# Optimization experiments

Measured on AMD Instinct MI355X. Metric: run time of the kernel, lower is better.

Reference implementation:

```python
import jax, jax.numpy as jnp
import numpy as np
import math

B, L, IN_DIM, OUT_DIM = 2, 2048, 128, 128
H, DH = 8, 32            # num_heads, dim_head
ED = H * DH * 2          # embed_dim = 512
DEPTH = 1
LAMBDA_INIT = 0.8 - 0.6 * math.exp(-0.3 * (DEPTH + 1))
EPS = 1e-8


def setup_inputs() -> dict:
    key = jax.random.key(0)
    ks = jax.random.split(key, 10)
    x = jax.random.normal(ks[0], (B, 1, L, IN_DIM), dtype=jnp.float32)
    mask_2d = jax.random.bernoulli(ks[1], 0.9, (B, L, L))
    Wq = jax.random.normal(ks[2], (IN_DIM, ED), dtype=jnp.float32) * 0.05
    Wkv = jax.random.normal(ks[3], (IN_DIM, 2 * ED), dtype=jnp.float32) * 0.05
    Wout = jax.random.normal(ks[4], (ED, OUT_DIM), dtype=jnp.float32) * 0.05
    lambda_q1 = jax.random.normal(ks[5], (DH,), dtype=jnp.float32) * 0.1
    lambda_k1 = jax.random.normal(ks[6], (DH,), dtype=jnp.float32) * 0.1
    lambda_q2 = jax.random.normal(ks[7], (DH,), dtype=jnp.float32) * 0.1
    lambda_k2 = jax.random.normal(ks[8], (DH,), dtype=jnp.float32) * 0.1
    gamma = jnp.ones((2 * DH,), dtype=jnp.float32)
    return {"x": x, "mask_2d": mask_2d, "Wq": Wq, "Wkv": Wkv, "Wout": Wout,
            "lambda_q1": lambda_q1, "lambda_k1": lambda_k1,
            "lambda_q2": lambda_q2, "lambda_k2": lambda_k2, "gamma": gamma}


def reference(x, mask_2d, Wq, Wkv, Wout, lambda_q1, lambda_k1, lambda_q2, lambda_k2, gamma):
    b = x.shape[0]
    xs = x[:, 0]                                   # [b, L, in_dim]
    q = xs @ Wq                                    # [b, L, 2*H*DH]
    k, v = jnp.split(xs @ Wkv, 2, axis=-1)
    q = q.reshape(b, L, 2 * H, DH).transpose(0, 2, 1, 3) * (DH ** -0.5)  # [b,2H,L,d]
    k = k.reshape(b, L, 2 * H, DH).transpose(0, 2, 1, 3)                 # [b,2H,L,d]
    v = v.reshape(b, L, H, 2 * DH).transpose(0, 2, 1, 3)                 # [b,H,L,2d]
    dots = jnp.einsum('bnld,bnmd->bnlm', q, k)     # [b,2H,L,L]
    mask_value = -jnp.finfo(dots.dtype).max
    dots = jnp.where(mask_2d[:, None, :, :], dots, mask_value)
    attn_w = jax.nn.softmax(dots.astype(jnp.float32), axis=-1).astype(dots.dtype)
    lam1 = jnp.exp(jnp.sum(lambda_q1 * lambda_k1))
    lam2 = jnp.exp(jnp.sum(lambda_q2 * lambda_k2))
    lam = lam1 - lam2 + LAMBDA_INIT
    attn_w = attn_w.reshape(b, H, 2, L, L)
    attn_w = attn_w[:, :, 0] - lam * attn_w[:, :, 1]   # [b,H,L,L]
    attn = jnp.einsum('bhlm,bhmd->bhld', attn_w, v)    # [b,H,L,2d]
    rms = jnp.sqrt(jnp.mean(attn ** 2, axis=-1, keepdims=True))
    attn = gamma * (attn / (rms + EPS)) * (1.0 - LAMBDA_INIT)
    out = attn.transpose(0, 2, 1, 3).reshape(b, L, H * 2 * DH) @ Wout  # [b,L,out_dim]
    return out[:, None]                             # [b,1,L,out_dim]
```

## Files before the change

### kernel.cpp

```cpp
#include <hip/hip_runtime.h>
#include <float.h>
#include <math.h>

typedef __attribute__((ext_vector_type(8))) short short8;
typedef __attribute__((ext_vector_type(4))) float f32x4;
typedef __attribute__((ext_vector_type(4))) unsigned short ushort4v;

constexpr int SEQL = 2048;
constexpr int NQH  = 16;
constexpr int NVH  = 8;
constexpr int DHD  = 32;
constexpr float LAMB_INIT = 0.4707130183436648f;
constexpr float REPS      = 1e-8f;
constexpr float QW        = 0.25503492f;

static __device__ __forceinline__ unsigned short f2bf(float f) {
    union { float f; unsigned u; } a; a.f = f;
    unsigned u = a.u;
    u += 0x7fffu + ((u >> 16) & 1u);
    return (unsigned short)(u >> 16);
}

static __device__ __forceinline__ unsigned cvtpk(float lo, float hi) {
    unsigned r;
    asm("v_cvt_pk_bf16_f32 %0, %1, %2" : "=v"(r) : "v"(lo), "v"(hi));
    return r;
}

static __device__ __forceinline__ float expv(float x) {
    float r;
    asm("v_exp_f32 %0, %1" : "=v"(r) : "v"(x));
    return r;
}

static __device__ __forceinline__ void stage16(const unsigned short* g, unsigned short* l) {
    __builtin_amdgcn_global_load_lds(
        (const __attribute__((address_space(1))) unsigned int*)g,
        (__attribute__((address_space(3))) unsigned int*)l, 16, 0, 0);
}

__global__ __launch_bounds__(256) void pack_prep_kernel(
        const unsigned char* __restrict__ mb, const int* __restrict__ mi,
        unsigned long long* __restrict__ bits,
        const float* __restrict__ x, const float* __restrict__ Wq,
        const float* __restrict__ Wkv, const float* __restrict__ Wout,
        unsigned short* __restrict__ xb, unsigned short* __restrict__ Wf,
        unsigned short* __restrict__ WfO) {
    __shared__ int cnt[256];
    int t = threadIdx.x;
    int c = 0;
    #pragma unroll
    for (int i = 0; i < 16; ++i) c += (mb[t * 16 + i] != 0);
    cnt[t] = c;
    __syncthreads();
    for (int s = 128; s > 0; s >>= 1) { if (t < s) cnt[t] += cnt[t + s]; __syncthreads(); }
    int f = cnt[0] > 2048;
    int gtid = blockIdx.x * 256 + t;
    int nthr = gridDim.x * 256;
    {
        const int total = 2 * SEQL * (SEQL / 64);
        int wid = blockIdx.x * 4 + (t >> 6);
        int lane = t & 63;
        int stride = gridDim.x * 4;
        for (int w = wid; w < total; w += stride) {
            int e = w * 64 + lane;
            int v = f ? (int)mb[e] : mi[e];
            unsigned long long b = __ballot(v != 0);
            if (lane == 0) bits[w] = b;
        }
    }
    {
        float4 v = ((const float4*)x)[gtid];
        ushort4v o = { f2bf(v.x), f2bf(v.y), f2bf(v.z), f2bf(v.w) };
        ((ushort4v*)xb)[gtid] = o;
    }
    for (int e = gtid; e < 262144; e += nthr) {
        int k = e >> 11, cc = e & 2047;
        if (cc < 1536) {
            float v = (cc < 512) ? Wq[(size_t)k * 512 + cc] * QW
                                 : Wkv[(size_t)k * 1024 + (cc - 512)];
            int cp = cc >> 4, lr = cc & 15, kk = k >> 5, lg = (k >> 3) & 3, j = k & 7;
            Wf[(((size_t)(cp * 4 + kk) * 4 + lg) * 16 + lr) * 8 + j] = f2bf(v);
        }
    }
    if (gtid < 65536) {
        int k = gtid >> 7, cc = gtid & 127;
        float v = Wout[gtid];
        int cp = cc >> 4, lr = cc & 15, kk = k >> 5, lg = (k >> 3) & 3, j = k & 7;
        WfO[(((size_t)(cp * 16 + kk) * 4 + lg) * 16 + lr) * 8 + j] = f2bf(v);
    }
}

__global__ __launch_bounds__(256) void qkv_mfma_kernel(
        const unsigned short* __restrict__ xb, const unsigned short* __restrict__ Wf,
        unsigned short* __restrict__ Q, unsigned short* __restrict__ Kf,
        unsigned short* __restrict__ Vf) {
    int t = threadIdx.x, w = t >> 6, lane = t & 63, lr = lane & 15, lg = lane >> 4;
    int lid = blockIdx.x;
    int swz = (lid & 7) * 192 + (lid >> 3);
    int by = swz >> 6, bx = swz & 63;
    int r0 = bx * 64 + w * 16;
    short8 ax[4];
    #pragma unroll
    for (int kk = 0; kk < 4; ++kk)
        ax[kk] = *(const short8*)(xb + (size_t)(r0 + lr) * 128 + kk * 32 + lg * 8);
    f32x4 acc[4];
    #pragma unroll
    for (int ct = 0; ct < 4; ++ct) acc[ct] = (f32x4){0.f, 0.f, 0.f, 0.f};
    #pragma unroll
    for (int ct = 0; ct < 4; ++ct) {
        int cp = by * 4 + ct;
        #pragma unroll
        for (int kk = 0; kk < 4; ++kk) {
            short8 bw = *(const short8*)(Wf + (size_t)(cp * 4 + kk) * 512 + lane * 8);
            acc[ct] = __builtin_amdgcn_mfma_f32_16x16x32_bf16(ax[kk], bw, acc[ct], 0, 0, 0);
        }
    }
    int gr0 = r0 + 4 * lg;
    int b = gr0 >> 11;
    if (by < 8) {
        #pragma unroll
        for (int ct = 0; ct < 4; ++ct) {
            int col = by * 64 + 16 * ct + lr;
            int n = col >> 5, d = col & 31;
            #pragma unroll
            for (int r = 0; r < 4; ++r) {
                int l = (gr0 + r) & 2047;
                Q[(((size_t)(b * NQH + n)) * SEQL + l) * DHD + d] = f2bf(acc[ct][r]);
            }
        }
    } else if (by < 16) {
        #pragma unroll
        for (int ct = 0; ct < 4; ++ct) {
            int ck = by * 64 + 16 * ct + lr - 512;
            int n = ck >> 5, dk = ck & 31;
            size_t hb = ((size_t)(b * NQH + n)) * 65536 + (dk >> 3) * 128 + (dk & 7);
            #pragma unroll
            for (int r = 0; r < 4; ++r) {
                int l = (gr0 + r) & 2047;
                Kf[hb + (size_t)((l >> 6) * 4 + ((l >> 4) & 3)) * 512 + (l & 15) * 8]
                    = f2bf(acc[ct][r]);
            }
        }
    } else {
        #pragma unroll
        for (int ct = 0; ct < 4; ++ct) {
            int cv = by * 64 + 16 * ct + lr - 1024;
            int h = cv >> 6, d = cv & 63;
            size_t hb = ((size_t)(b * NVH + h)) * 131072 + (d >> 4) * 512 + (d & 15) * 8;
            #pragma unroll
            for (int r = 0; r < 4; ++r) {
                int l = (gr0 + r) & 2047;
                Vf[hb + (size_t)((l >> 6) * 2 + ((l >> 5) & 1)) * 2048
                      + ((l >> 4) & 1) * 4 + ((l >> 2) & 3) * 128 + (l & 3)]
                    = f2bf(acc[ct][r]);
            }
        }
    }
}

__global__ __launch_bounds__(512, 2) void attn_kernel(
        const unsigned short* __restrict__ Q, const unsigned short* __restrict__ Kf,
        const unsigned short* __restrict__ Vf, const unsigned long long* __restrict__ bits,
        const float* __restrict__ lq1, const float* __restrict__ lk1,
        const float* __restrict__ lq2, const float* __restrict__ lk2,
        const float* __restrict__ gamma, unsigned short* __restrict__ Ab) {
    __shared__ unsigned short lds[3][8192];
    int tid = threadIdx.x;
    int w = tid >> 6, lane = tid & 63;
    int lr = lane & 15, lg = lane >> 4;
    int ws = w & 3, hh = w >> 2;
    int lid = blockIdx.y * 32 + blockIdx.x;
    int swz = (lid & 7) * 64 + (lid >> 3);
    int qtile = swz & 31, bp = swz >> 5;
    int b = bp >> 3, h = bp & 7;
    int q0 = qtile * 64 + ws * 16;
    int bnA = b * NQH + 2 * h;
    int bn = bnA + hh;

    short8 aq = *(const short8*)(Q + (((size_t)bn) * SEQL + q0 + lr) * DHD + lg * 8);
    const unsigned short* KH2 = Kf + ((size_t)bnA) * 65536;
    const unsigned short* VH  = Vf + ((size_t)(b * NVH + h)) * 131072;
    const unsigned long long* mrow = bits + ((size_t)b * SEQL + q0 + lr) * 32;

    auto stage_tile = [&](int bf, int it) {
        #pragma unroll
        for (int j = 0; j < 2; ++j) {
            int c = 2 * w + j;
            const unsigned short* src =
                (c < 4) ? (KH2 + (size_t)it * 2048 + c * 512)
              : (c < 8) ? (KH2 + 65536 + (size_t)it * 2048 + (c - 4) * 512)
                        : (VH + (size_t)it * 4096 + (c - 8) * 512);
            stage16(src + lane * 8, &lds[bf][c * 512]);
        }
    };

    f32x4 oacc[4];
    #pragma unroll
    for (int m = 0; m < 4; ++m) oacc[m] = (f32x4){0.f, 0.f, 0.f, 0.f};
    float ssum = 0.f;
    const f32x4 Z = {0.f, 0.f, 0.f, 0.f};

    stage_tile(0, 0);
    stage_tile(1, 1);
    unsigned long long mw = mrow[0];

    for (int t = 0; t < 32; ++t) {
        asm volatile("s_waitcnt vmcnt(3)" ::: "memory");
        __builtin_amdgcn_s_barrier();
        __builtin_amdgcn_sched_barrier(0);
        stage_tile((t + 2) % 3, (t + 2) & 31);
        unsigned long long mwc = mw;
        mw = mrow[(t + 1) & 31];
        __builtin_amdgcn_sched_barrier(0);
        const unsigned short* L = &lds[t % 3][0];
        short8 bk[4], bv[8];
        #pragma unroll
        for (int c = 0; c < 4; ++c)
            bk[c] = *(const short8*)(L + hh * 2048 + c * 512 + lane * 8);
        #pragma unroll
        for (int z = 0; z < 8; ++z)
            bv[z] = *(const short8*)(L + 4096 + z * 512 + lane * 8);
        f32x4 s[4];
        __builtin_amdgcn_s_setprio(1);
        #pragma unroll
        for (int c = 0; c < 4; ++c)
            s[c] = __builtin_amdgcn_mfma_f32_16x16x32_bf16(bk[c], aq, Z, 0, 0, 0);
        __builtin_amdgcn_s_setprio(0);
        unsigned long long mwl = mwc >> (4 * lg);
        unsigned mlo = (unsigned)mwl, mhi = (unsigned)(mwl >> 32);
        float p[4][4];
        #pragma unroll
        for (int c = 0; c < 4; ++c) {
            unsigned wv = (c < 2) ? mlo : mhi;
            int sh = (c & 1) * 16;
            #pragma unroll
            for (int r = 0; r < 4; ++r) {
                unsigned keep = (wv >> (sh + r)) & 1u;
                float e = expv(s[c][r]);
                p[c][r] = keep ? e : 0.f;
            }
        }
        float ac = 0.f;
        #pragma unroll
        for (int c = 0; c < 4; ++c)
            #pragma unroll
            for (int r = 0; r < 4; ++r) ac += p[c][r];
        ssum += ac;
        union { short8 v; unsigned u[4]; } a0, a1;
        a0.u[0] = cvtpk(p[0][0], p[0][1]); a0.u[1] = cvtpk(p[0][2], p[0][3]);
        a0.u[2] = cvtpk(p[1][0], p[1][1]); a0.u[3] = cvtpk(p[1][2], p[1][3]);
        a1.u[0] = cvtpk(p[2][0], p[2][1]); a1.u[1] = cvtpk(p[2][2], p[2][3]);
        a1.u[2] = cvtpk(p[3][0], p[3][1]); a1.u[3] = cvtpk(p[3][2], p[3][3]);
        __builtin_amdgcn_s_setprio(1);
        #pragma unroll
        for (int m = 0; m < 4; ++m)
            oacc[m] = __builtin_amdgcn_mfma_f32_16x16x32_bf16(a0.v, bv[m], oacc[m], 0, 0, 0);
        #pragma unroll
        for (int m = 0; m < 4; ++m)
            oacc[m] = __builtin_amdgcn_mfma_f32_16x16x32_bf16(a1.v, bv[4 + m], oacc[m], 0, 0, 0);
        __builtin_amdgcn_s_setprio(0);
    }
    asm volatile("s_waitcnt vmcnt(0)" ::: "memory");
    __syncthreads();
    ssum += __shfl_xor(ssum, 16, 64);
    ssum += __shfl_xor(ssum, 32, 64);
    float inv = 1.f / ssum;
    float invr[4];
    #pragma unroll
    for (int r = 0; r < 4; ++r) invr[r] = __shfl(inv, 4 * lg + r, 64);
    float on[4][4];
    #pragma unroll
    for (int m = 0; m < 4; ++m)
        #pragma unroll
        for (int r = 0; r < 4; ++r) on[m][r] = oacc[m][r] * invr[r];
    float* fb = (float*)&lds[0][0];
    if (hh) {
        #pragma unroll
        for (int m = 0; m < 4; ++m)
            #pragma unroll
            for (int r = 0; r < 4; ++r)
                fb[ws * 1088 + lane * 17 + m * 4 + r] = on[m][r];
    }
    __syncthreads();
    if (hh) return;
    int l31 = lane & 31;
    float t1 = lq1[l31] * lk1[l31];
    float t2 = lq2[l31] * lk2[l31];
    #pragma unroll
    for (int o = 1; o < 32; o <<= 1) { t1 += __shfl_xor(t1, o, 64); t2 += __shfl_xor(t2, o, 64); }
    float lam = __expf(t1) - __expf(t2) + LAMB_INIT;
    float dv[4][4];
    float sq[4] = {0.f, 0.f, 0.f, 0.f};
    #pragma unroll
    for (int m = 0; m < 4; ++m)
        #pragma unroll
        for (int r = 0; r < 4; ++r) {
            float v = on[m][r] - lam * fb[ws * 1088 + lane * 17 + m * 4 + r];
            dv[m][r] = v;
            sq[r] += v * v;
        }
    #pragma unroll
    for (int r = 0; r < 4; ++r) {
        #pragma unroll
        for (int o = 1; o < 16; o <<= 1) sq[r] += __shfl_xor(sq[r], o, 64);
        sq[r] = (1.f - LAMB_INIT) / (sqrtf(sq[r] * (1.f / 64.f)) + REPS);
    }
    float gm[4];
    #pragma unroll
    for (int m = 0; m < 4; ++m) gm[m] = gamma[16 * m + lr];
    unsigned short* Abp = Ab + ((size_t)(b * SEQL + q0 + 4 * lg)) * 512 + h * 64 + lr;
    #pragma unroll
    for (int m = 0; m < 4; ++m)
        #pragma unroll
        for (int r = 0; r < 4; ++r)
            Abp[(size_t)r * 512 + 16 * m] = f2bf(dv[m][r] * sq[r] * gm[m]);
}

__global__ __launch_bounds__(64) void proj_mfma_kernel(
        const unsigned short* __restrict__ Ab, const unsigned short* __restrict__ WfO,
        float* __restrict__ out) {
    int lane = threadIdx.x & 63, lr = lane & 15, lg = lane >> 4;
    int r0 = blockIdx.x * 16;
    f32x4 acc[8];
    #pragma unroll
    for (int ct = 0; ct < 8; ++ct) acc[ct] = (f32x4){0.f, 0.f, 0.f, 0.f};
    #pragma unroll
    for (int kk = 0; kk < 16; ++kk) {
        short8 af = *(const short8*)(Ab + (size_t)(r0 + lr) * 512 + kk * 32 + lg * 8);
        #pragma unroll
        for (int ct = 0; ct < 8; ++ct) {
            short8 bf = *(const short8*)(WfO + (size_t)(ct * 16 + kk) * 512 + lane * 8);
            acc[ct] = __builtin_amdgcn_mfma_f32_16x16x32_bf16(af, bf, acc[ct], 0, 0, 0);
        }
    }
    #pragma unroll
    for (int ct = 0; ct < 8; ++ct)
        #pragma unroll
        for (int r = 0; r < 4; ++r)
            out[(size_t)(r0 + 4 * lg + r) * 128 + ct * 16 + lr] = acc[ct][r];
}

extern "C" void kernel_launch(void* const* d_in, const int* in_sizes, int n_in,
                              void* d_out, int out_size, void* d_ws, size_t ws_size,
                              hipStream_t stream) {
    const float* x    = (const float*)d_in[0];
    const void*  mask = d_in[1];
    const float* Wq   = (const float*)d_in[2];
    const float* Wkv  = (const float*)d_in[3];
    const float* Wout = (const float*)d_in[4];
    const float* lq1  = (const float*)d_in[5];
    const float* lk1  = (const float*)d_in[6];
    const float* lq2  = (const float*)d_in[7];
    const float* lk2  = (const float*)d_in[8];
    const float* gam  = (const float*)d_in[9];
    float* out = (float*)d_out;

    char* wsb = (char*)d_ws;
    unsigned long long* bits = (unsigned long long*)(wsb + 4096);
    unsigned short* Q        = (unsigned short*)(wsb + 1052672);
    unsigned short* Kf       = (unsigned short*)(wsb + 5246976);
    unsigned short* Vf       = (unsigned short*)(wsb + 9441280);
    unsigned short* xb       = (unsigned short*)(wsb + 13635584);
    unsigned short* Wf       = (unsigned short*)(wsb + 14684160);
    unsigned short* WfO      = (unsigned short*)(wsb + 15077376);
    unsigned short* Ab       = (unsigned short*)(wsb + 15208448);

    pack_prep_kernel<<<512, 256, 0, stream>>>((const unsigned char*)mask,
                                              (const int*)mask, bits,
                                              x, Wq, Wkv, Wout, xb, Wf, WfO);
    qkv_mfma_kernel<<<1536, 256, 0, stream>>>(xb, Wf, Q, Kf, Vf);
    attn_kernel<<<dim3(32, 16), 512, 0, stream>>>(Q, Kf, Vf, bits,
                                                  lq1, lk1, lq2, lk2, gam, Ab);
    proj_mfma_kernel<<<256, 64, 0, stream>>>(Ab, WfO, out);
}
```

Measured before the change: 96.72 us.

## Halve attention block to 4 waves, each processing two 16-row query tiles

```diff
diff --git a/kernel.cpp b/kernel.cpp
--- a/kernel.cpp
+++ b/kernel.cpp
@@ -159,7 +159,7 @@
     }
 }
 
-__global__ __launch_bounds__(512, 2) void attn_kernel(
+__global__ __launch_bounds__(256, 2) void attn_kernel(
         const unsigned short* __restrict__ Q, const unsigned short* __restrict__ Kf,
         const unsigned short* __restrict__ Vf, const unsigned long long* __restrict__ bits,
         const float* __restrict__ lq1, const float* __restrict__ lk1,
@@ -169,51 +169,58 @@
     int tid = threadIdx.x;
     int w = tid >> 6, lane = tid & 63;
     int lr = lane & 15, lg = lane >> 4;
-    int ws = w & 3, hh = w >> 2;
+    int ws = w & 1, hh = w >> 1;
     int lid = blockIdx.y * 32 + blockIdx.x;
     int swz = (lid & 7) * 64 + (lid >> 3);
     int qtile = swz & 31, bp = swz >> 5;
     int b = bp >> 3, h = bp & 7;
-    int q0 = qtile * 64 + ws * 16;
+    int q0 = qtile * 64 + ws * 32;
     int bnA = b * NQH + 2 * h;
     int bn = bnA + hh;
 
-    short8 aq = *(const short8*)(Q + (((size_t)bn) * SEQL + q0 + lr) * DHD + lg * 8);
+    short8 aq0 = *(const short8*)(Q + (((size_t)bn) * SEQL + q0 + lr) * DHD + lg * 8);
+    short8 aq1 = *(const short8*)(Q + (((size_t)bn) * SEQL + q0 + 16 + lr) * DHD + lg * 8);
     const unsigned short* KH2 = Kf + ((size_t)bnA) * 65536;
     const unsigned short* VH  = Vf + ((size_t)(b * NVH + h)) * 131072;
-    const unsigned long long* mrow = bits + ((size_t)b * SEQL + q0 + lr) * 32;
+    const unsigned long long* mrow0 = bits + ((size_t)b * SEQL + q0 + lr) * 32;
+    const unsigned long long* mrow1 = mrow0 + 16 * 32;
+
+    const unsigned short* gsrc;
+    int gstride;
+    if (w == 0)      { gsrc = KH2;         gstride = 2048; }
+    else if (w == 1) { gsrc = KH2 + 65536; gstride = 2048; }
+    else if (w == 2) { gsrc = VH;          gstride = 4096; }
+    else             { gsrc = VH + 2048;   gstride = 4096; }
+    const unsigned short* gl = gsrc + lane * 8;
+    const int ldso = w * 2048;
 
     auto stage_tile = [&](int bf, int it) {
         #pragma unroll
-        for (int j = 0; j < 2; ++j) {
-            int c = 2 * w + j;
-            const unsigned short* src =
-                (c < 4) ? (KH2 + (size_t)it * 2048 + c * 512)
-              : (c < 8) ? (KH2 + 65536 + (size_t)it * 2048 + (c - 4) * 512)
-                        : (VH + (size_t)it * 4096 + (c - 8) * 512);
-            stage16(src + lane * 8, &lds[bf][c * 512]);
-        }
+        for (int j = 0; j < 4; ++j)
+            stage16(gl + (size_t)it * gstride + j * 512, &lds[bf][ldso + j * 512]);
     };
 
-    f32x4 oacc[4];
-    #pragma unroll
-    for (int m = 0; m < 4; ++m) oacc[m] = (f32x4){0.f, 0.f, 0.f, 0.f};
-    float ssum = 0.f;
+    f32x4 o0[4], o1[4];
+    #pragma unroll
+    for (int m = 0; m < 4; ++m) { o0[m] = (f32x4){0,0,0,0}; o1[m] = (f32x4){0,0,0,0}; }
+    float ss0 = 0.f, ss1 = 0.f;
     const f32x4 Z = {0.f, 0.f, 0.f, 0.f};
 
     stage_tile(0, 0);
+    unsigned long long mw0 = mrow0[0];
+    unsigned long long mw1 = mrow1[0];
     stage_tile(1, 1);
-    unsigned long long mw = mrow[0];
-
-    for (int t = 0; t < 32; ++t) {
-        asm volatile("s_waitcnt vmcnt(3)" ::: "memory");
+
+    auto body = [&](int t, int cur, int nx, bool do_stage) {
+        asm volatile("s_waitcnt vmcnt(6)" ::: "memory");
         __builtin_amdgcn_s_barrier();
         __builtin_amdgcn_sched_barrier(0);
-        stage_tile((t + 2) % 3, (t + 2) & 31);
-        unsigned long long mwc = mw;
-        mw = mrow[(t + 1) & 31];
+        if (do_stage) stage_tile(nx, (t + 2) & 31);
+        unsigned long long m0c = mw0, m1c = mw1;
+        mw0 = mrow0[(t + 1) & 31];
+        mw1 = mrow1[(t + 1) & 31];
         __builtin_amdgcn_sched_barrier(0);
-        const unsigned short* L = &lds[t % 3][0];
+        const unsigned short* L = &lds[cur][0];
         short8 bk[4], bv[8];
         #pragma unroll
         for (int c = 0; c < 4; ++c)
@@ -221,66 +228,99 @@
         #pragma unroll
         for (int z = 0; z < 8; ++z)
             bv[z] = *(const short8*)(L + 4096 + z * 512 + lane * 8);
-        f32x4 s[4];
+        f32x4 s0[4], s1[4];
         __builtin_amdgcn_s_setprio(1);
         #pragma unroll
         for (int c = 0; c < 4; ++c)
-            s[c] = __builtin_amdgcn_mfma_f32_16x16x32_bf16(bk[c], aq, Z, 0, 0, 0);
+            s0[c] = __builtin_amdgcn_mfma_f32_16x16x32_bf16(bk[c], aq0, Z, 0, 0, 0);
+        #pragma unroll
+        for (int c = 0; c < 4; ++c)
+            s1[c] = __builtin_amdgcn_mfma_f32_16x16x32_bf16(bk[c], aq1, Z, 0, 0, 0);
         __builtin_amdgcn_s_setprio(0);
-        unsigned long long mwl = mwc >> (4 * lg);
-        unsigned mlo = (unsigned)mwl, mhi = (unsigned)(mwl >> 32);
-        float p[4][4];
+        unsigned long long l0 = m0c >> (4 * lg), l1 = m1c >> (4 * lg);
+        unsigned lo0 = (unsigned)l0, hi0 = (unsigned)(l0 >> 32);
+        unsigned lo1 = (unsigned)l1, hi1 = (unsigned)(l1 >> 32);
+        float p0[4][4], p1[4][4];
         #pragma unroll
         for (int c = 0; c < 4; ++c) {
-            unsigned wv = (c < 2) ? mlo : mhi;
+            unsigned wv0 = (c < 2) ? lo0 : hi0;
+            unsigned wv1 = (c < 2) ? lo1 : hi1;
             int sh = (c & 1) * 16;
             #pragma unroll
             for (int r = 0; r < 4; ++r) {
-                unsigned keep = (wv >> (sh + r)) & 1u;
-                float e = expv(s[c][r]);
-                p[c][r] = keep ? e : 0.f;
+                unsigned k0 = (wv0 >> (sh + r)) & 1u;
+                unsigned k1 = (wv1 >> (sh + r)) & 1u;
+                float e0 = expv(s0[c][r]);
+                float e1 = expv(s1[c][r]);
+                p0[c][r] = k0 ? e0 : 0.f;
+                p1[c][r] = k1 ? e1 : 0.f;
             }
         }
-        float ac = 0.f;
+        float a0s = 0.f, a1s = 0.f;
         #pragma unroll
         for (int c = 0; c < 4; ++c)
             #pragma unroll
-            for (int r = 0; r < 4; ++r) ac += p[c][r];
-        ssum += ac;
-        union { short8 v; unsigned u[4]; } a0, a1;
-        a0.u[0] = cvtpk(p[0][0], p[0][1]); a0.u[1] = cvtpk(p[0][2], p[0][3]);
-        a0.u[2] = cvtpk(p[1][0], p[1][1]); a0.u[3] = cvtpk(p[1][2], p[1][3]);
-        a1.u[0] = cvtpk(p[2][0], p[2][1]); a1.u[1] = cvtpk(p[2][2], p[2][3]);
-        a1.u[2] = cvtpk(p[3][0], p[3][1]); a1.u[3] = cvtpk(p[3][2], p[3][3]);
+            for (int r = 0; r < 4; ++r) { a0s += p0[c][r]; a1s += p1[c][r]; }
+        ss0 += a0s; ss1 += a1s;
+        union { short8 v; unsigned u[4]; } x00, x01, x10, x11;
+        x00.u[0] = cvtpk(p0[0][0], p0[0][1]); x00.u[1] = cvtpk(p0[0][2], p0[0][3]);
+        x00.u[2] = cvtpk(p0[1][0], p0[1][1]); x00.u[3] = cvtpk(p0[1][2], p0[1][3]);
+        x01.u[0] = cvtpk(p0[2][0], p0[2][1]); x01.u[1] = cvtpk(p0[2][2], p0[2][3]);
+        x01.u[2] = cvtpk(p0[3][0], p0[3][1]); x01.u[3] = cvtpk(p0[3][2], p0[3][3]);
+        x10.u[0] = cvtpk(p1[0][0], p1[0][1]); x10.u[1] = cvtpk(p1[0][2], p1[0][3]);
+        x10.u[2] = cvtpk(p1[1][0], p1[1][1]); x10.u[3] = cvtpk(p1[1][2], p1[1][3]);
+        x11.u[0] = cvtpk(p1[2][0], p1[2][1]); x11.u[1] = cvtpk(p1[2][2], p1[2][3]);
+        x11.u[2] = cvtpk(p1[3][0], p1[3][1]); x11.u[3] = cvtpk(p1[3][2], p1[3][3]);
         __builtin_amdgcn_s_setprio(1);
         #pragma unroll
-        for (int m = 0; m < 4; ++m)
-            oacc[m] = __builtin_amdgcn_mfma_f32_16x16x32_bf16(a0.v, bv[m], oacc[m], 0, 0, 0);
-        #pragma unroll
-        for (int m = 0; m < 4; ++m)
-            oacc[m] = __builtin_amdgcn_mfma_f32_16x16x32_bf16(a1.v, bv[4 + m], oacc[m], 0, 0, 0);
+        for (int m = 0; m < 4; ++m) {
+            o0[m] = __builtin_amdgcn_mfma_f32_16x16x32_bf16(x00.v, bv[m], o0[m], 0, 0, 0);
+            o1[m] = __builtin_amdgcn_mfma_f32_16x16x32_bf16(x10.v, bv[m], o1[m], 0, 0, 0);
+        }
+        #pragma unroll
+        for (int m = 0; m < 4; ++m) {
+            o0[m] = __builtin_amdgcn_mfma_f32_16x16x32_bf16(x01.v, bv[4 + m], o0[m], 0, 0, 0);
+            o1[m] = __builtin_amdgcn_mfma_f32_16x16x32_bf16(x11.v, bv[4 + m], o1[m], 0, 0, 0);
+        }
         __builtin_amdgcn_s_setprio(0);
-    }
+    };
+
+    for (int tb = 0; tb < 30; tb += 3) {
+        body(tb + 0, 0, 2, true);
+        body(tb + 1, 1, 0, true);
+        body(tb + 2, 2, 1, true);
+    }
+    body(30, 0, 2, true);
+    body(31, 1, 0, false);
+
     asm volatile("s_waitcnt vmcnt(0)" ::: "memory");
     __syncthreads();
-    ssum += __shfl_xor(ssum, 16, 64);
-    ssum += __shfl_xor(ssum, 32, 64);
-    float inv = 1.f / ssum;
-    float invr[4];
-    #pragma unroll
-    for (int r = 0; r < 4; ++r) invr[r] = __shfl(inv, 4 * lg + r, 64);
-    float on[4][4];
+    ss0 += __shfl_xor(ss0, 16, 64); ss0 += __shfl_xor(ss0, 32, 64);
+    ss1 += __shfl_xor(ss1, 16, 64); ss1 += __shfl_xor(ss1, 32, 64);
+    float inv0 = 1.f / ss0, inv1 = 1.f / ss1;
+    float i0[4], i1[4];
+    #pragma unroll
+    for (int r = 0; r < 4; ++r) {
+        i0[r] = __shfl(inv0, 4 * lg + r, 64);
+        i1[r] = __shfl(inv1, 4 * lg + r, 64);
+    }
+    float on0[4][4], on1[4][4];
     #pragma unroll
     for (int m = 0; m < 4; ++m)
         #pragma unroll
-        for (int r = 0; r < 4; ++r) on[m][r] = oacc[m][r] * invr[r];
+        for (int r = 0; r < 4; ++r) {
+            on0[m][r] = o0[m][r] * i0[r];
+            on1[m][r] = o1[m][r] * i1[r];
+        }
     float* fb = (float*)&lds[0][0];
     if (hh) {
         #pragma unroll
         for (int m = 0; m < 4; ++m)
             #pragma unroll
-            for (int r = 0; r < 4; ++r)
-                fb[ws * 1088 + lane * 17 + m * 4 + r] = on[m][r];
+            for (int r = 0; r < 4; ++r) {
+                fb[ws * 2048 + (m * 4 + r) * 64 + lane]        = on0[m][r];
+                fb[ws * 2048 + (16 + m * 4 + r) * 64 + lane]   = on1[m][r];
+            }
     }
     __syncthreads();
     if (hh) return;
@@ -290,21 +330,26 @@
     #pragma unroll
     for (int o = 1; o < 32; o <<= 1) { t1 += __shfl_xor(t1, o, 64); t2 += __shfl_xor(t2, o, 64); }
     float lam = __expf(t1) - __expf(t2) + LAMB_INIT;
-    float dv[4][4];
-    float sq[4] = {0.f, 0.f, 0.f, 0.f};
+    float dv0[4][4], dv1[4][4];
+    float sq0[4] = {0.f, 0.f, 0.f, 0.f}, sq1[4] = {0.f, 0.f, 0.f, 0.f};
     #pragma unroll
     for (int m = 0; m < 4; ++m)
         #pragma unroll
         for (int r = 0; r < 4; ++r) {
-            float v = on[m][r] - lam * fb[ws * 1088 + lane * 17 + m * 4 + r];
-            dv[m][r] = v;
-            sq[r] += v * v;
+            float v0 = on0[m][r] - lam * fb[ws * 2048 + (m * 4 + r) * 64 + lane];
+            float v1 = on1[m][r] - lam * fb[ws * 2048 + (16 + m * 4 + r) * 64 + lane];
+            dv0[m][r] = v0; sq0[r] += v0 * v0;
+            dv1[m][r] = v1; sq1[r] += v1 * v1;
         }
     #pragma unroll
     for (int r = 0; r < 4; ++r) {
         #pragma unroll
-        for (int o = 1; o < 16; o <<= 1) sq[r] += __shfl_xor(sq[r], o, 64);
-        sq[r] = (1.f - LAMB_INIT) / (sqrtf(sq[r] * (1.f / 64.f)) + REPS);
+        for (int o = 1; o < 16; o <<= 1) {
+            sq0[r] += __shfl_xor(sq0[r], o, 64);
+            sq1[r] += __shfl_xor(sq1[r], o, 64);
+        }
+        sq0[r] = (1.f - LAMB_INIT) / (sqrtf(sq0[r] * (1.f / 64.f)) + REPS);
+        sq1[r] = (1.f - LAMB_INIT) / (sqrtf(sq1[r] * (1.f / 64.f)) + REPS);
     }
     float gm[4];
     #pragma unroll
@@ -313,8 +358,10 @@
     #pragma unroll
     for (int m = 0; m < 4; ++m)
         #pragma unroll
-        for (int r = 0; r < 4; ++r)
-            Abp[(size_t)r * 512 + 16 * m] = f2bf(dv[m][r] * sq[r] * gm[m]);
+        for (int r = 0; r < 4; ++r) {
+            Abp[(size_t)r * 512 + 16 * m]        = f2bf(dv0[m][r] * sq0[r] * gm[m]);
+            Abp[(size_t)(16 + r) * 512 + 16 * m] = f2bf(dv1[m][r] * sq1[r] * gm[m]);
+        }
 }
 
 __global__ __launch_bounds__(64) void proj_mfma_kernel(
@@ -370,7 +417,7 @@
                                               (const int*)mask, bits,
                                               x, Wq, Wkv, Wout, xb, Wf, WfO);
     qkv_mfma_kernel<<<1536, 256, 0, stream>>>(xb, Wf, Q, Kf, Vf);
-    attn_kernel<<<dim3(32, 16), 512, 0, stream>>>(Q, Kf, Vf, bits,
+    attn_kernel<<<dim3(32, 16), 256, 0, stream>>>(Q, Kf, Vf, bits,
                                                   lq1, lk1, lq2, lk2, gam, Ab);
     proj_mfma_kernel<<<256, 64, 0, stream>>>(Ab, WfO, out);
 }
```

After: 98.41 us. No clear change (+1.8%).

## Drop LDS staging in attention, load K/V directly to registers; split-K projection

Applied to the files above, without the earlier changes.

```diff
diff --git a/kernel.cpp b/kernel.cpp
--- a/kernel.cpp
+++ b/kernel.cpp
@@ -31,12 +31,6 @@
     float r;
     asm("v_exp_f32 %0, %1" : "=v"(r) : "v"(x));
     return r;
-}
-
-static __device__ __forceinline__ void stage16(const unsigned short* g, unsigned short* l) {
-    __builtin_amdgcn_global_load_lds(
-        (const __attribute__((address_space(1))) unsigned int*)g,
-        (__attribute__((address_space(3))) unsigned int*)l, 16, 0, 0);
 }
 
 __global__ __launch_bounds__(256) void pack_prep_kernel(
@@ -159,41 +153,29 @@
     }
 }
 
-__global__ __launch_bounds__(512, 2) void attn_kernel(
+__global__ __launch_bounds__(256, 3) void attn_kernel(
         const unsigned short* __restrict__ Q, const unsigned short* __restrict__ Kf,
         const unsigned short* __restrict__ Vf, const unsigned long long* __restrict__ bits,
         const float* __restrict__ lq1, const float* __restrict__ lk1,
         const float* __restrict__ lq2, const float* __restrict__ lk2,
         const float* __restrict__ gamma, unsigned short* __restrict__ Ab) {
-    __shared__ unsigned short lds[3][8192];
+    __shared__ float fb[2048];
     int tid = threadIdx.x;
     int w = tid >> 6, lane = tid & 63;
     int lr = lane & 15, lg = lane >> 4;
-    int ws = w & 3, hh = w >> 2;
-    int lid = blockIdx.y * 32 + blockIdx.x;
-    int swz = (lid & 7) * 64 + (lid >> 3);
-    int qtile = swz & 31, bp = swz >> 5;
+    int ws = w & 1, hh = w >> 1;
+    int lid = blockIdx.y * 64 + blockIdx.x;
+    int swz = (lid & 7) * 128 + (lid >> 3);
+    int qtile = swz & 63, bp = swz >> 6;
     int b = bp >> 3, h = bp & 7;
-    int q0 = qtile * 64 + ws * 16;
+    int q0 = qtile * 32 + ws * 16;
     int bnA = b * NQH + 2 * h;
     int bn = bnA + hh;
 
     short8 aq = *(const short8*)(Q + (((size_t)bn) * SEQL + q0 + lr) * DHD + lg * 8);
-    const unsigned short* KH2 = Kf + ((size_t)bnA) * 65536;
-    const unsigned short* VH  = Vf + ((size_t)(b * NVH + h)) * 131072;
+    const unsigned short* KH = Kf + ((size_t)bn) * 65536;
+    const unsigned short* VH = Vf + ((size_t)(b * NVH + h)) * 131072;
     const unsigned long long* mrow = bits + ((size_t)b * SEQL + q0 + lr) * 32;
-
-    auto stage_tile = [&](int bf, int it) {
-        #pragma unroll
-        for (int j = 0; j < 2; ++j) {
-            int c = 2 * w + j;
-            const unsigned short* src =
-                (c < 4) ? (KH2 + (size_t)it * 2048 + c * 512)
-              : (c < 8) ? (KH2 + 65536 + (size_t)it * 2048 + (c - 4) * 512)
-                        : (VH + (size_t)it * 4096 + (c - 8) * 512);
-            stage16(src + lane * 8, &lds[bf][c * 512]);
-        }
-    };
 
     f32x4 oacc[4];
     #pragma unroll
@@ -201,31 +183,29 @@
     float ssum = 0.f;
     const f32x4 Z = {0.f, 0.f, 0.f, 0.f};
 
-    stage_tile(0, 0);
-    stage_tile(1, 1);
+    short8 bkE[4], bkO[4];
+    #pragma unroll
+    for (int c = 0; c < 4; ++c)
+        bkE[c] = *(const short8*)(KH + c * 512 + lane * 8);
     unsigned long long mw = mrow[0];
 
-    for (int t = 0; t < 32; ++t) {
-        asm volatile("s_waitcnt vmcnt(3)" ::: "memory");
-        __builtin_amdgcn_s_barrier();
-        __builtin_amdgcn_sched_barrier(0);
-        stage_tile((t + 2) % 3, (t + 2) & 31);
+    auto body = [&](int t, short8* bkc, short8* bkn) {
         unsigned long long mwc = mw;
         mw = mrow[(t + 1) & 31];
-        __builtin_amdgcn_sched_barrier(0);
-        const unsigned short* L = &lds[t % 3][0];
-        short8 bk[4], bv[8];
+        const unsigned short* KT = KH + (size_t)((t + 1) & 31) * 2048;
         #pragma unroll
         for (int c = 0; c < 4; ++c)
-            bk[c] = *(const short8*)(L + hh * 2048 + c * 512 + lane * 8);
+            bkn[c] = *(const short8*)(KT + c * 512 + lane * 8);
+        const unsigned short* VT = VH + (size_t)t * 4096;
+        short8 bv[8];
         #pragma unroll
         for (int z = 0; z < 8; ++z)
-            bv[z] = *(const short8*)(L + 4096 + z * 512 + lane * 8);
+            bv[z] = *(const short8*)(VT + z * 512 + lane * 8);
         f32x4 s[4];
         __builtin_amdgcn_s_setprio(1);
         #pragma unroll
         for (int c = 0; c < 4; ++c)
-            s[c] = __builtin_amdgcn_mfma_f32_16x16x32_bf16(bk[c], aq, Z, 0, 0, 0);
+            s[c] = __builtin_amdgcn_mfma_f32_16x16x32_bf16(bkc[c], aq, Z, 0, 0, 0);
         __builtin_amdgcn_s_setprio(0);
         unsigned long long mwl = mwc >> (4 * lg);
         unsigned mlo = (unsigned)mwl, mhi = (unsigned)(mwl >> 32);
@@ -260,9 +240,13 @@
         for (int m = 0; m < 4; ++m)
             oacc[m] = __builtin_amdgcn_mfma_f32_16x16x32_bf16(a1.v, bv[4 + m], oacc[m], 0, 0, 0);
         __builtin_amdgcn_s_setprio(0);
-    }
-    asm volatile("s_waitcnt vmcnt(0)" ::: "memory");
-    __syncthreads();
+    };
+
+    for (int tp = 0; tp < 16; ++tp) {
+        body(2 * tp,     bkE, bkO);
+        body(2 * tp + 1, bkO, bkE);
+    }
+
     ssum += __shfl_xor(ssum, 16, 64);
     ssum += __shfl_xor(ssum, 32, 64);
     float inv = 1.f / ssum;
@@ -274,13 +258,12 @@
     for (int m = 0; m < 4; ++m)
         #pragma unroll
         for (int r = 0; r < 4; ++r) on[m][r] = oacc[m][r] * invr[r];
-    float* fb = (float*)&lds[0][0];
     if (hh) {
         #pragma unroll
         for (int m = 0; m < 4; ++m)
             #pragma unroll
             for (int r = 0; r < 4; ++r)
-                fb[ws * 1088 + lane * 17 + m * 4 + r] = on[m][r];
+                fb[ws * 1024 + (m * 4 + r) * 64 + lane] = on[m][r];
     }
     __syncthreads();
     if (hh) return;
@@ -296,7 +279,7 @@
     for (int m = 0; m < 4; ++m)
         #pragma unroll
         for (int r = 0; r < 4; ++r) {
-            float v = on[m][r] - lam * fb[ws * 1088 + lane * 17 + m * 4 + r];
+            float v = on[m][r] - lam * fb[ws * 1024 + (m * 4 + r) * 64 + lane];
             dv[m][r] = v;
             sq[r] += v * v;
         }
@@ -317,16 +300,18 @@
             Abp[(size_t)r * 512 + 16 * m] = f2bf(dv[m][r] * sq[r] * gm[m]);
 }
 
-__global__ __launch_bounds__(64) void proj_mfma_kernel(
+__global__ __launch_bounds__(256) void proj_mfma_kernel(
         const unsigned short* __restrict__ Ab, const unsigned short* __restrict__ WfO,
         float* __restrict__ out) {
-    int lane = threadIdx.x & 63, lr = lane & 15, lg = lane >> 4;
+    __shared__ f32x4 red[1536];
+    int t = threadIdx.x, w = t >> 6, lane = t & 63, lr = lane & 15, lg = lane >> 4;
     int r0 = blockIdx.x * 16;
     f32x4 acc[8];
     #pragma unroll
     for (int ct = 0; ct < 8; ++ct) acc[ct] = (f32x4){0.f, 0.f, 0.f, 0.f};
     #pragma unroll
-    for (int kk = 0; kk < 16; ++kk) {
+    for (int j = 0; j < 4; ++j) {
+        int kk = w * 4 + j;
         short8 af = *(const short8*)(Ab + (size_t)(r0 + lr) * 512 + kk * 32 + lg * 8);
         #pragma unroll
         for (int ct = 0; ct < 8; ++ct) {
@@ -334,11 +319,25 @@
             acc[ct] = __builtin_amdgcn_mfma_f32_16x16x32_bf16(af, bf, acc[ct], 0, 0, 0);
         }
     }
-    #pragma unroll
-    for (int ct = 0; ct < 8; ++ct)
+    if (w) {
+        #pragma unroll
+        for (int ct = 0; ct < 8; ++ct)
+            red[((w - 1) * 8 + ct) * 64 + lane] = acc[ct];
+    }
+    __syncthreads();
+    if (w) return;
+    #pragma unroll
+    for (int ct = 0; ct < 8; ++ct) {
+        #pragma unroll
+        for (int j = 0; j < 3; ++j) {
+            f32x4 pv = red[(j * 8 + ct) * 64 + lane];
+            acc[ct][0] += pv[0]; acc[ct][1] += pv[1];
+            acc[ct][2] += pv[2]; acc[ct][3] += pv[3];
+        }
         #pragma unroll
         for (int r = 0; r < 4; ++r)
             out[(size_t)(r0 + 4 * lg + r) * 128 + ct * 16 + lr] = acc[ct][r];
+    }
 }
 
 extern "C" void kernel_launch(void* const* d_in, const int* in_sizes, int n_in,
@@ -370,7 +369,7 @@
                                               (const int*)mask, bits,
                                               x, Wq, Wkv, Wout, xb, Wf, WfO);
     qkv_mfma_kernel<<<1536, 256, 0, stream>>>(xb, Wf, Q, Kf, Vf);
-    attn_kernel<<<dim3(32, 16), 512, 0, stream>>>(Q, Kf, Vf, bits,
+    attn_kernel<<<dim3(64, 16), 256, 0, stream>>>(Q, Kf, Vf, bits,
                                                   lq1, lk1, lq2, lk2, gam, Ab);
-    proj_mfma_kernel<<<256, 64, 0, stream>>>(Ab, WfO, out);
-}
+    proj_mfma_kernel<<<256, 256, 0, stream>>>(Ab, WfO, out);
+}
```

Result: slower. 110.6 us (+14.3%).
